# Optimization experiments

Measured on AMD Instinct MI355X. Metric: run time of the kernel, lower is better.

## Reference

```python
import jax, jax.numpy as jnp
import numpy as np

TEXT_VOCAB = 32000
NUM_CODEBOOKS = 8
CODEBOOK_SIZE = 1024
SLICE = CODEBOOK_SIZE + 2  # codebook slice length incl. BOS/EOS
AUDIO_VOCAB = NUM_CODEBOOKS * SLICE  # 8208
HIDDEN = 2048
NH = 16
NKV = 8
HD = HIDDEN // NH  # 128
FFN = 8192
LAYERS = 2
EPS = 1e-5


def setup_inputs() -> dict:
    key = jax.random.key(0)
    ks = jax.random.split(key, 16)
    s = 0.02
    qkv_dim = (NH + 2 * NKV) * HD  # 4096
    inp = {
        "input_ids": jax.random.randint(ks[0], (2, 1024), 0, TEXT_VOCAB + CODEBOOK_SIZE, dtype=jnp.int32),
        "vocab_embed": jax.random.normal(ks[1], (TEXT_VOCAB, HIDDEN), jnp.float32) * s,
        "audio_embed": jax.random.normal(ks[2], (AUDIO_VOCAB, HIDDEN), jnp.float32) * s,
        "ln_in": jnp.ones((LAYERS, HIDDEN), jnp.float32),
        "ln_audio_in": jnp.ones((LAYERS, HIDDEN), jnp.float32),
        "ln_post": jnp.ones((LAYERS, HIDDEN), jnp.float32),
        "ln_audio_post": jnp.ones((LAYERS, HIDDEN), jnp.float32),
        "w_qkv": jax.random.normal(ks[3], (LAYERS, HIDDEN, qkv_dim), jnp.float32) * s,
        "w_o": jax.random.normal(ks[4], (LAYERS, NH * HD, HIDDEN), jnp.float32) * s,
        "w_fc": jax.random.normal(ks[5], (LAYERS, HIDDEN, FFN), jnp.float32) * s,
        "w_proj": jax.random.normal(ks[6], (LAYERS, FFN, HIDDEN), jnp.float32) * s,
        "w_audio_fc": jax.random.normal(ks[7], (LAYERS, HIDDEN, FFN), jnp.float32) * s,
        "w_audio_proj": jax.random.normal(ks[8], (LAYERS, FFN, HIDDEN), jnp.float32) * s,
        "ln_f": jnp.ones((HIDDEN,), jnp.float32),
    }
    return inp


def _rms(x, w):
    return x * jax.lax.rsqrt(jnp.mean(x * x, axis=-1, keepdims=True) + EPS) * w


def reference(input_ids, vocab_embed, audio_embed, ln_in, ln_audio_in, ln_post,
              ln_audio_post, w_qkv, w_o, w_fc, w_proj, w_audio_fc, w_audio_proj, ln_f):
    B, S = input_ids.shape
    audio_mask = input_ids > TEXT_VOCAB - 1  # [B,S] bool
    mask3 = audio_mask[..., None]

    # --- embedding ---
    text_ids = jnp.where(audio_mask, TEXT_VOCAB - 1, input_ids)
    text_e = vocab_embed[text_ids]  # [B,S,H]
    audio_ids = jnp.where(audio_mask, input_ids - TEXT_VOCAB, 0)
    shift = jnp.arange(NUM_CODEBOOKS, dtype=jnp.int32) * SLICE  # [C]
    audio_e = audio_embed[audio_ids[None] + shift[:, None, None]].sum(0)  # [B,S,H]
    h = jnp.where(mask3, audio_e, text_e)

    causal = jnp.tril(jnp.ones((S, S), bool))
    scale = 1.0 / np.sqrt(HD)

    def layer(h, p):
        li, lai, lp, lap, wqkv, wo, wfc, wpr, wafc, wapr = p
        # dual-path input norm (both computed, merged by mask)
        x = jnp.where(mask3, _rms(h, lai), _rms(h, li))
        # causal GQA attention
        qkv = x @ wqkv
        q = qkv[..., : NH * HD].reshape(B, S, NH, HD)
        k = qkv[..., NH * HD:(NH + NKV) * HD].reshape(B, S, NKV, HD)
        v = qkv[..., (NH + NKV) * HD:].reshape(B, S, NKV, HD)
        rep = NH // NKV
        k = jnp.repeat(k, rep, axis=2)
        v = jnp.repeat(v, rep, axis=2)
        scores = jnp.einsum('bqhd,bkhd->bhqk', q, k) * scale
        scores = jnp.where(causal, scores, jnp.finfo(scores.dtype).min)
        attn = jax.nn.softmax(scores, axis=-1)
        o = jnp.einsum('bhqk,bkhd->bqhd', attn, v).reshape(B, S, NH * HD) @ wo
        h = h + o
        # dual-path FFN (both computed, merged by mask)
        y_text = jax.nn.silu(_rms(h, lp) @ wfc) @ wpr
        y_audio = jax.nn.silu(_rms(h, lap) @ wafc) @ wapr
        h = h + jnp.where(mask3, y_audio, y_text)
        return h, None

    params = (ln_in, ln_audio_in, ln_post, ln_audio_post,
              w_qkv, w_o, w_fc, w_proj, w_audio_fc, w_audio_proj)
    h, _ = jax.lax.scan(layer, h, params)
    return _rms(h, ln_f)
```

## Files before the change

### kernel.cpp

```cpp
#include <hip/hip_runtime.h>
#include <hip/hip_bf16.h>

typedef unsigned short u16;
typedef __attribute__((ext_vector_type(4))) float f32x4;
typedef __attribute__((ext_vector_type(8))) short bf16x8;
typedef __attribute__((ext_vector_type(8))) unsigned short u16x8;
typedef __attribute__((ext_vector_type(4))) unsigned short u16x4;

#define BM 128
#define BN 128
#define BK 64

__device__ __forceinline__ u16 f2bf(float f) {
  union { float f; unsigned u; } v; v.f = f;
  unsigned r = v.u + 0x7FFFu + ((v.u >> 16) & 1u);
  return (u16)(r >> 16);
}
__device__ __forceinline__ float bf2f(u16 v) {
  union { float f; unsigned u; } x; x.u = (unsigned)v << 16; return x.f;
}

__device__ __forceinline__ int xswz(int wg, int n) {
  return (wg & 7) * (n >> 3) + (wg >> 3);
}

__device__ __forceinline__ void g8_stage_half(
    const u16* __restrict__ G, int ldg, int tile, int half, u16* ldsbase) {
  const int tid = threadIdx.x;
#pragma unroll
  for (int load = 0; load < 2; ++load) {
    int unit = load * 512 + tid;
    int row = unit >> 3;
    int seg = (unit & 7) ^ ((unit >> 3) & 7);
    __builtin_amdgcn_global_load_lds(
        (const __attribute__((address_space(1))) void*)(G + (size_t)(half * 128 + row) * ldg + tile * 64 + seg * 8),
        (__attribute__((address_space(3))) void*)(ldsbase + half * 8192 + load * 4096 + (tid >> 6) * 512),
        16, 0, 0);
  }
}

__device__ __forceinline__ void g8_core(
    const u16* __restrict__ A, int lda, const u16* __restrict__ Bt, int ldb,
    int NT, u16* lds, f32x4 acc[8][4]) {
  const int tid = threadIdx.x;
  const int lane = tid & 63;
  const int wid = tid >> 6;
  const int wr = wid >> 2, wc = wid & 3;
  const int lr = lane & 15;
  const int lk4 = lane >> 4;
  const int sw = lane & 7;
  const int off0 = ((lk4 ^ sw) * 8);
  const int off1 = (((4 + lk4) ^ sw) * 8);

  u16* ldsA = lds;
  u16* ldsB = lds + 32768;

  g8_stage_half(A, lda, 0, 0, ldsA);
  g8_stage_half(A, lda, 0, 1, ldsA);
  g8_stage_half(Bt, ldb, 0, 0, ldsB);
  g8_stage_half(Bt, ldb, 0, 1, ldsB);
  if (NT > 1) {
    g8_stage_half(Bt, ldb, 1, 0, ldsB + 16384);
    g8_stage_half(Bt, ldb, 1, 1, ldsB + 16384);
  }
  asm volatile("s_waitcnt vmcnt(4)" ::: "memory");
  __builtin_amdgcn_s_barrier();
  __builtin_amdgcn_sched_barrier(0);

  for (int g = 0; g < NT; ++g) {
    const int buf = g & 1;
    const u16* cA = ldsA + buf * 16384 + wr * 8192;
    const u16* cB = ldsB + buf * 16384;
    bf16x8 bv[4][2];
#pragma unroll
    for (int p = 0; p < 4; ++p) {
      bf16x8 av[2][2];
      if (p == 0) {
#pragma unroll
        for (int n = 0; n < 4; ++n) {
          int rg = wc * 64 + n * 16 + lr;
          const u16* rbase = &cB[(rg >> 7) * 8192 + (rg & 127) * 64];
          bv[n][0] = *(const bf16x8*)&rbase[off0];
          bv[n][1] = *(const bf16x8*)&rbase[off1];
        }
      }
#pragma unroll
      for (int m2 = 0; m2 < 2; ++m2) {
        const u16* rbase = &cA[((p * 2 + m2) * 16 + lr) * 64];
        av[m2][0] = *(const bf16x8*)&rbase[off0];
        av[m2][1] = *(const bf16x8*)&rbase[off1];
      }

      if (p == 0 && g + 1 < NT) g8_stage_half(A, lda, g + 1, 0, ldsA + ((g + 1) & 1) * 16384);
      if (p == 1 && g + 1 < NT) g8_stage_half(A, lda, g + 1, 1, ldsA + ((g + 1) & 1) * 16384);
      if (p == 2 && g + 2 < NT) g8_stage_half(Bt, ldb, g + 2, 0, ldsB + buf * 16384);
      if (p == 3) {
        if (g + 2 < NT) {
          g8_stage_half(Bt, ldb, g + 2, 1, ldsB + buf * 16384);
          asm volatile("s_waitcnt vmcnt(4)" ::: "memory");
        } else if (g + 1 < NT) {
          asm volatile("s_waitcnt vmcnt(0)" ::: "memory");
        }
      }
      __builtin_amdgcn_s_barrier();
      asm volatile("s_waitcnt lgkmcnt(0)" ::: "memory");
      __builtin_amdgcn_sched_barrier(0);
      __builtin_amdgcn_s_setprio(1);
#pragma unroll
      for (int m2 = 0; m2 < 2; ++m2)
#pragma unroll
        for (int n = 0; n < 4; ++n)
#pragma unroll
          for (int kk = 0; kk < 2; ++kk)
            acc[p * 2 + m2][n] = __builtin_amdgcn_mfma_f32_16x16x32_bf16(
                av[m2][kk], bv[n][kk], acc[p * 2 + m2][n], 0, 0, 0);
      __builtin_amdgcn_s_setprio(0);
      __builtin_amdgcn_sched_barrier(0);
      __builtin_amdgcn_s_barrier();
    }
  }
}

__device__ __forceinline__ void g8_acc_zero(f32x4 acc[8][4]) {
#pragma unroll
  for (int m = 0; m < 8; ++m)
#pragma unroll
    for (int n = 0; n < 4; ++n)
      acc[m][n] = (f32x4){0.f, 0.f, 0.f, 0.f};
}

__global__ __launch_bounds__(512, 2) void k_gemm8_qkv(
    const u16* __restrict__ A, const u16* __restrict__ Bt, u16* __restrict__ Pq) {
  __shared__ u16 lds[65536];
  const int wg = xswz(blockIdx.x, 256);
  const int ks = wg >> 7, rem = wg & 127;
  const int tm = rem >> 4, tn = rem & 15;
  f32x4 acc[8][4];
  g8_acc_zero(acc);
  g8_core(A + (size_t)tm * 256 * 2048 + ks * 1024, 2048,
          Bt + (size_t)tn * 256 * 2048 + ks * 1024, 2048, 16, lds, acc);
  const int lane = threadIdx.x & 63, wid = threadIdx.x >> 6;
  const int wr = wid >> 2, wc = wid & 3;
  const int col = lane & 15, rb = (lane >> 4) * 4;
#pragma unroll
  for (int m = 0; m < 8; ++m)
#pragma unroll
    for (int n = 0; n < 4; ++n)
#pragma unroll
      for (int j = 0; j < 4; ++j) {
        int gm = tm * 256 + wr * 128 + m * 16 + rb + j;
        int gn = tn * 256 + wc * 64 + n * 16 + col;
        Pq[((size_t)ks * 2048 + gm) * 4096 + gn] = f2bf(acc[m][n][j]);
      }
}

__global__ __launch_bounds__(512, 2) void k_gemm8_fc(
    const u16* __restrict__ A, const u16* __restrict__ Bt, u16* __restrict__ Cb) {
  __shared__ u16 lds[65536];
  const int wg = xswz(blockIdx.x, 256);
  const int tm = wg >> 5, tn = wg & 31;
  f32x4 acc[8][4];
  g8_acc_zero(acc);
  g8_core(A + (size_t)tm * 256 * 2048, 2048, Bt + (size_t)tn * 256 * 2048, 2048, 32, lds, acc);
  const int lane = threadIdx.x & 63, wid = threadIdx.x >> 6;
  const int wr = wid >> 2, wc = wid & 3;
  const int col = lane & 15, rb = (lane >> 4) * 4;
#pragma unroll
  for (int m = 0; m < 8; ++m)
#pragma unroll
    for (int n = 0; n < 4; ++n)
#pragma unroll
      for (int j = 0; j < 4; ++j) {
        int gm = tm * 256 + wr * 128 + m * 16 + rb + j;
        int gn = tn * 256 + wc * 64 + n * 16 + col;
        float v = acc[m][n][j];
        Cb[(size_t)gm * 8192 + gn] = f2bf(v / (1.f + __expf(-v)));
      }
}

__global__ __launch_bounds__(512, 2) void k_gemm8_sk(
    const u16* __restrict__ A, int lda, const u16* __restrict__ Bt, int ldb,
    int NT, int koff, u16* __restrict__ Pp) {
  __shared__ u16 lds[65536];
  const int wg = xswz(blockIdx.x, 256);
  const int ks = wg >> 6, rem = wg & 63;
  const int tm = rem >> 3, tn = rem & 7;
  f32x4 acc[8][4];
  g8_acc_zero(acc);
  g8_core(A + (size_t)tm * 256 * lda + ks * koff, lda,
          Bt + (size_t)tn * 256 * ldb + ks * koff, ldb, NT, lds, acc);
  const int lane = threadIdx.x & 63, wid = threadIdx.x >> 6;
  const int wr = wid >> 2, wc = wid & 3;
  const int col = lane & 15, rb = (lane >> 4) * 4;
#pragma unroll
  for (int m = 0; m < 8; ++m)
#pragma unroll
    for (int n = 0; n < 4; ++n)
#pragma unroll
      for (int j = 0; j < 4; ++j) {
        int gm = tm * 256 + wr * 128 + m * 16 + rb + j;
        int gn = tn * 256 + wc * 64 + n * 16 + col;
        Pp[((size_t)ks * 2048 + gm) * 2048 + gn] = f2bf(acc[m][n][j]);
      }
}

__global__ __launch_bounds__(256) void k_red_qkv(
    const u16* __restrict__ Pq, u16* __restrict__ Q, u16* __restrict__ Kb,
    u16* __restrict__ VT) {
  const int gm = blockIdx.y;
  const int c = blockIdx.x * 1024 + threadIdx.x * 4;
  const size_t i = (size_t)gm * 4096 + c;
  u16x4 a = *(const u16x4*)&Pq[i];
  u16x4 b2 = *(const u16x4*)&Pq[(size_t)2048 * 4096 + i];
  const int b = gm >> 10, s = gm & 1023;
  u16 v[4];
#pragma unroll
  for (int j = 0; j < 4; ++j) v[j] = f2bf(bf2f(a[j]) + bf2f(b2[j]));
  const int d = c & 127;
  if (c < 2048) {
    int hh = c >> 7;
    *(u16x4*)&Q[((size_t)((b * 16 + hh) * 1024 + s)) * 128 + d] = *(u16x4*)v;
  } else if (c < 3072) {
    int kv = (c - 2048) >> 7;
    *(u16x4*)&Kb[((size_t)((b * 8 + kv) * 1024 + s)) * 128 + d] = *(u16x4*)v;
  } else {
    int kv = (c - 3072) >> 7;
#pragma unroll
    for (int j = 0; j < 4; ++j)
      VT[((size_t)((b * 8 + kv) * 128 + d + j)) * 1024 + s] = v[j];
  }
}

__device__ __forceinline__ void fa_stage128(const u16* __restrict__ G, int ldg, u16* dst,
                                            int nloads) {
  const int tid = threadIdx.x;
  for (int ld = 0; ld < nloads; ++ld) {
    int unit = ld * 256 + tid;
    int row = unit >> 4;
    int seg = (unit & 15) ^ (row & 7);
    __builtin_amdgcn_global_load_lds(
        (const __attribute__((address_space(1))) void*)(G + (size_t)row * ldg + seg * 8),
        (__attribute__((address_space(3))) void*)(dst + ld * 2048 + (tid >> 6) * 512),
        16, 0, 0);
  }
}
__device__ __forceinline__ void fa_stage64(const u16* __restrict__ G, int ldg, u16* dst,
                                           int nloads) {
  const int tid = threadIdx.x;
  for (int ld = 0; ld < nloads; ++ld) {
    int unit = ld * 256 + tid;
    int row = unit >> 3;
    int seg = (unit & 7) ^ (row & 7);
    __builtin_amdgcn_global_load_lds(
        (const __attribute__((address_space(1))) void*)(G + (size_t)row * ldg + seg * 8),
        (__attribute__((address_space(3))) void*)(dst + ld * 2048 + (tid >> 6) * 512),
        16, 0, 0);
  }
}

__global__ __launch_bounds__(256, 2) void k_fattn(
    const u16* __restrict__ Q, const u16* __restrict__ Kb, const u16* __restrict__ VT,
    u16* __restrict__ O) {
  const int tm = blockIdx.x;
  const int bh = blockIdx.y;
  const int b = bh >> 4, hq = bh & 15, kv = hq >> 1;
  __shared__ u16 lds[32768];
  u16* Klds = lds;
  u16* Vlds = lds + 8192;
  u16* Plds = lds + 24576;
  const int lane = threadIdx.x & 63, wave = threadIdx.x >> 6;
  const int wm = wave * 32;
  const int lr = lane & 15, lk = lane >> 4;
  const int rb = lk * 4;
  const int cl = lr;

  const u16* Qg = Q + ((size_t)(b * 16 + hq) * 1024 + tm * 128) * 128;
  fa_stage128(Qg, 128, lds, 8);
  asm volatile("s_waitcnt vmcnt(0)" ::: "memory");
  __builtin_amdgcn_s_barrier();
  __builtin_amdgcn_sched_barrier(0);
  bf16x8 qf[2][4];
#pragma unroll
  for (int m = 0; m < 2; ++m)
#pragma unroll
    for (int kk = 0; kk < 4; ++kk) {
      int row = wm + m * 16 + lr;
      qf[m][kk] = *(const bf16x8*)&lds[row * 128 + (((kk * 4 + lk) ^ (lr & 7)) * 8)];
    }
  asm volatile("s_waitcnt lgkmcnt(0)" ::: "memory");
  __builtin_amdgcn_s_barrier();
  __builtin_amdgcn_sched_barrier(0);

  const u16* Kg = Kb + (size_t)(b * 8 + kv) * 1024 * 128;
  const u16* Vg = VT + (size_t)(b * 8 + kv) * 128 * 1024;
  const int NT = 2 * (tm + 1);
  fa_stage128(Kg, 128, Klds, 4);
  fa_stage64(Vg, 1024, Vlds, 4);

  f32x4 accO[2][8];
#pragma unroll
  for (int m = 0; m < 2; ++m)
#pragma unroll
    for (int n = 0; n < 8; ++n) accO[m][n] = (f32x4){0.f, 0.f, 0.f, 0.f};
  float mst[8], lst[8];
#pragma unroll
  for (int i = 0; i < 8; ++i) { mst[i] = -3.0e38f; lst[i] = 0.f; }
  const float scale = 0.08838834764831845f;

  for (int t = 0; t < NT; ++t) {
    asm volatile("s_waitcnt vmcnt(0)" ::: "memory");
    __builtin_amdgcn_s_barrier();
    __builtin_amdgcn_sched_barrier(0);
    u16* Vcur = Vlds + (t & 1) * 8192;
    f32x4 accS[2][4];
#pragma unroll
    for (int m = 0; m < 2; ++m)
#pragma unroll
      for (int n = 0; n < 4; ++n) accS[m][n] = (f32x4){0.f, 0.f, 0.f, 0.f};
#pragma unroll
    for (int kk = 0; kk < 4; ++kk) {
      bf16x8 kf[4];
#pragma unroll
      for (int n = 0; n < 4; ++n)
        kf[n] = *(const bf16x8*)&Klds[(n * 16 + lr) * 128 + (((kk * 4 + lk) ^ (lr & 7)) * 8)];
#pragma unroll
      for (int m = 0; m < 2; ++m)
#pragma unroll
        for (int n = 0; n < 4; ++n)
          accS[m][n] = __builtin_amdgcn_mfma_f32_16x16x32_bf16(qf[m][kk], kf[n], accS[m][n], 0, 0, 0);
    }
    asm volatile("s_waitcnt lgkmcnt(0)" ::: "memory");
    __builtin_amdgcn_s_barrier();
    __builtin_amdgcn_sched_barrier(0);
    if (t + 1 < NT) {
      fa_stage128(Kg + (size_t)(t + 1) * 64 * 128, 128, Klds, 4);
      fa_stage64(Vg + (t + 1) * 64, 1024, Vlds + ((t + 1) & 1) * 8192, 4);
    }
    const bool dm = (t >= 2 * tm);
#pragma unroll
    for (int m = 0; m < 2; ++m)
#pragma unroll
      for (int j = 0; j < 4; ++j) {
        const int si = m * 4 + j;
        const int rglob = tm * 128 + wm + m * 16 + rb + j;
        float v[4];
        float vmax = -3.0e38f;
#pragma unroll
        for (int n = 0; n < 4; ++n) {
          float x = accS[m][n][j] * scale;
          if (dm && (t * 64 + n * 16 + cl > rglob)) x = -3.0e38f;
          v[n] = x;
          vmax = fmaxf(vmax, x);
        }
#pragma unroll
        for (int o = 1; o < 16; o <<= 1) vmax = fmaxf(vmax, __shfl_xor(vmax, o));
        float mnew = fmaxf(mst[si], vmax);
        float alpha = __expf(mst[si] - mnew);
        mst[si] = mnew;
        float rs = 0.f;
        const int prow = wm + m * 16 + rb + j;
#pragma unroll
        for (int n = 0; n < 4; ++n) {
          float pp = __expf(v[n] - mnew);
          rs += pp;
          int col = n * 16 + cl;
          Plds[prow * 64 + (((col >> 3) ^ (prow & 7)) * 8) + (col & 7)] = f2bf(pp);
        }
#pragma unroll
        for (int o = 1; o < 16; o <<= 1) rs += __shfl_xor(rs, o);
        lst[si] = lst[si] * alpha + rs;
#pragma unroll
        for (int n = 0; n < 8; ++n) accO[m][n][j] *= alpha;
      }
#pragma unroll
    for (int kk = 0; kk < 2; ++kk) {
      bf16x8 pf[2], vf[8];
#pragma unroll
      for (int m = 0; m < 2; ++m) {
        int prow = wm + m * 16 + lr;
        pf[m] = *(const bf16x8*)&Plds[prow * 64 + (((kk * 4 + lk) ^ (lr & 7)) * 8)];
      }
#pragma unroll
      for (int n = 0; n < 8; ++n) {
        int d = n * 16 + lr;
        vf[n] = *(const bf16x8*)&Vcur[d * 64 + (((kk * 4 + lk) ^ (d & 7)) * 8)];
      }
#pragma unroll
      for (int m = 0; m < 2; ++m)
#pragma unroll
        for (int n = 0; n < 8; ++n)
          accO[m][n] = __builtin_amdgcn_mfma_f32_16x16x32_bf16(pf[m], vf[n], accO[m][n], 0, 0, 0);
    }
  }
#pragma unroll
  for (int m = 0; m < 2; ++m)
#pragma unroll
    for (int j = 0; j < 4; ++j) {
      float invl = 1.f / lst[m * 4 + j];
      int s = tm * 128 + wm + m * 16 + rb + j;
#pragma unroll
      for (int n = 0; n < 8; ++n) {
        int d = n * 16 + cl;
        O[(size_t)(b * 1024 + s) * 2048 + hq * 128 + d] = f2bf(accO[m][n][j] * invl);
      }
    }
}

__device__ __forceinline__ void acc_zero(f32x4 acc[4][4]) {
#pragma unroll
  for (int m = 0; m < 4; ++m)
#pragma unroll
    for (int n = 0; n < 4; ++n)
      acc[m][n] = (f32x4){0.f, 0.f, 0.f, 0.f};
}

__global__ __launch_bounds__(256) void k_gemm_csf(
    const u16* __restrict__ A, int lda, const float* __restrict__ Wf, int ldw,
    int ksteps, int ntn, u16* __restrict__ Pp, const int* __restrict__ cnt) {
  const int Na = cnt[0];
  const int tm = blockIdx.y;
  if (tm * 128 >= Na) return;
  const int tn = blockIdx.x % ntn;
  const int ks = blockIdx.x / ntn;
  const int ldc = ntn * 128;
  const int k0 = ks * ksteps * BK;
  __shared__ u16 sA[2 * BM * BK], sB[2 * BN * BK];
  f32x4 acc[4][4];
  acc_zero(acc);

  const u16* Ab = A + (size_t)tm * 128 * lda + k0;
  const float* Wb = Wf + (size_t)k0 * ldw + tn * 128;

  const int tid = threadIdx.x;
  const int wave = tid >> 6, lane = tid & 63;
  const int r = tid >> 3;
  const int ksw = (tid & 7) ^ ((tid >> 3) & 7);
  const int wm = (wave >> 1) * 64, wn = (wave & 1) * 64;
  const int lr = lane & 15, lk4 = lane >> 4, sw = lane & 7;
  const int off0 = ((lk4 ^ sw) * 8), off1 = (((4 + lk4) ^ sw) * 8);
  const int amax = Na - 1 - tm * 128;
  const int bk_ = tid >> 5;
  const int bn4 = (tid & 31) * 4;

  f32x4 breg[8];

  auto stageA = [&](int buf, int kt) {
    u16* dA = sA + buf * 8192 + wave * 512;
    const int kk0 = kt * BK;
#pragma unroll
    for (int i = 0; i < 4; ++i) {
      int ra = i * 32 + r; if (ra > amax) ra = amax;
      __builtin_amdgcn_global_load_lds(
          (const __attribute__((address_space(1))) void*)(Ab + (size_t)ra * lda + kk0 + ksw * 8),
          (__attribute__((address_space(3))) void*)(dA + i * 2048), 16, 0, 0);
    }
  };
  auto loadB = [&](int kt) {
#pragma unroll
    for (int i = 0; i < 8; ++i) {
      int kk_ = kt * 64 + i * 8 + bk_;
      breg[i] = __builtin_nontemporal_load((const f32x4*)&Wb[(size_t)kk_ * ldw + bn4]);
    }
  };
  auto writeB = [&](int buf) {
    u16* dB = sB + buf * 8192;
#pragma unroll
    for (int i = 0; i < 8; ++i) {
      int kk_ = i * 8 + bk_;
#pragma unroll
      for (int j = 0; j < 4; ++j) {
        int n = bn4 + j;
        dB[n * 64 + (((kk_ >> 3) ^ (n & 7)) * 8) + (kk_ & 7)] = f2bf(breg[i][j]);
      }
    }
  };

  stageA(0, 0);
  loadB(0);
  asm volatile("s_waitcnt vmcnt(0)" ::: "memory");
  writeB(0);
  asm volatile("s_waitcnt lgkmcnt(0)" ::: "memory");
  __builtin_amdgcn_s_barrier();
  __builtin_amdgcn_sched_barrier(0);

  for (int kt = 0; kt < ksteps; ++kt) {
    const int cur = kt & 1;
    if (kt + 1 < ksteps) { stageA(cur ^ 1, kt + 1); loadB(kt + 1); }
    const u16* cA = sA + cur * 8192;
    const u16* cB = sB + cur * 8192;
#pragma unroll
    for (int kk = 0; kk < 2; ++kk) {
      const int off = kk ? off1 : off0;
      bf16x8 av[4], bv[4];
#pragma unroll
      for (int m = 0; m < 4; ++m)
        av[m] = *(const bf16x8*)&cA[(wm + m * 16 + lr) * BK + off];
#pragma unroll
      for (int n = 0; n < 4; ++n)
        bv[n] = *(const bf16x8*)&cB[(wn + n * 16 + lr) * BK + off];
#pragma unroll
      for (int m = 0; m < 4; ++m)
#pragma unroll
        for (int n = 0; n < 4; ++n)
          acc[m][n] = __builtin_amdgcn_mfma_f32_16x16x32_bf16(av[m], bv[n], acc[m][n], 0, 0, 0);
    }
    asm volatile("s_waitcnt vmcnt(0)" ::: "memory");
    if (kt + 1 < ksteps) writeB(cur ^ 1);
    asm volatile("s_waitcnt lgkmcnt(0)" ::: "memory");
    __builtin_amdgcn_s_barrier();
    __builtin_amdgcn_sched_barrier(0);
  }

  const int col = lane & 15, rb = (lane >> 4) * 4;
#pragma unroll
  for (int m = 0; m < 4; ++m)
#pragma unroll
    for (int n = 0; n < 4; ++n)
#pragma unroll
      for (int j = 0; j < 4; ++j) {
        int gm = tm * 128 + wm + m * 16 + rb + j;
        int gn = tn * 128 + wn + n * 16 + col;
        Pp[((size_t)ks * 256 + gm) * ldc + gn] = f2bf(acc[m][n][j]);
      }
}

__global__ __launch_bounds__(256) void k_red8_silu(
    const u16* __restrict__ Pp, u16* __restrict__ t1, const int* __restrict__ cnt) {
  const int row = blockIdx.y;
  if (row >= cnt[0]) return;
  const int c = blockIdx.x * 1024 + threadIdx.x * 4;
  const size_t i = (size_t)row * 8192 + c;
  float s[4] = {0.f, 0.f, 0.f, 0.f};
#pragma unroll
  for (int k = 0; k < 8; ++k) {
    u16x4 a = *(const u16x4*)&Pp[(size_t)k * 256 * 8192 + i];
#pragma unroll
    for (int j = 0; j < 4; ++j) s[j] += bf2f(a[j]);
  }
  u16x4 ov;
#pragma unroll
  for (int j = 0; j < 4; ++j) {
    float v = s[j];
    ov[j] = f2bf(v / (1.f + __expf(-v)));
  }
  *(u16x4*)&t1[i] = ov;
}

__device__ __forceinline__ float block_sum256(float v, float* red) {
  const int tid = threadIdx.x;
#pragma unroll
  for (int o = 32; o; o >>= 1) v += __shfl_xor(v, o);
  if ((tid & 63) == 0) red[tid >> 6] = v;
  __syncthreads();
  float r = red[0] + red[1] + red[2] + red[3];
  __syncthreads();
  return r;
}

__global__ __launch_bounds__(256) void k_trans_embed(
    const float* __restrict__ w_qkv, const float* __restrict__ w_o,
    const float* __restrict__ w_fc, const float* __restrict__ w_proj,
    u16* __restrict__ WtAll,
    const int* __restrict__ ids, const float* __restrict__ vocab,
    const float* __restrict__ audio, const float* __restrict__ wt,
    const float* __restrict__ wa, float* __restrict__ h, int* __restrict__ mask,
    u16* __restrict__ x) {
  __shared__ float tile[64][65];
  const int tid = threadIdx.x;
  if (blockIdx.x < 22528) {
    int bid = blockIdx.x;
    int l = 0;
    if (bid >= 11264) { l = 1; bid -= 11264; }
    const float* src;
    u16* dst;
    int K, N, t;
    u16* WtL = WtAll + (size_t)l * 46137344;
    if (bid < 2048)       { src = w_qkv  + (size_t)l * 8388608;  dst = WtL;            K = 2048; N = 4096; t = bid; }
    else if (bid < 3072)  { src = w_o    + (size_t)l * 4194304;  dst = WtL + 8388608;  K = 2048; N = 2048; t = bid - 2048; }
    else if (bid < 7168)  { src = w_fc   + (size_t)l * 16777216; dst = WtL + 12582912; K = 2048; N = 8192; t = bid - 3072; }
    else                  { src = w_proj + (size_t)l * 16777216; dst = WtL + 29360128; K = 8192; N = 2048; t = bid - 7168; }
    const int nk = K >> 6;
    const int sb = t >> 6, w = t & 63;
    const int nsbk = nk >> 3;
    const int tk = ((sb % nsbk) << 3) + (w & 7);
    const int tn = ((sb / nsbk) << 3) + (w >> 3);
#pragma unroll
    for (int i = 0; i < 4; ++i) {
      int idx = i * 256 + tid;
      int r = idx >> 4, c4 = (idx & 15) * 4;
      f32x4 v = __builtin_nontemporal_load(
          (const f32x4*)&src[(size_t)(tk * 64 + r) * N + tn * 64 + c4]);
      tile[r][c4]     = v[0];
      tile[r][c4 + 1] = v[1];
      tile[r][c4 + 2] = v[2];
      tile[r][c4 + 3] = v[3];
    }
    __syncthreads();
#pragma unroll
    for (int i = 0; i < 2; ++i) {
      int u = i * 256 + tid;
      int n = u >> 3, seg = u & 7;
      u16x8 ov;
#pragma unroll
      for (int j = 0; j < 8; ++j) ov[j] = f2bf(tile[seg * 8 + j][n]);
      __builtin_nontemporal_store(ov,
          (u16x8*)&dst[(size_t)(tn * 64 + n) * K + tk * 64 + seg * 8]);
    }
  } else {
    const int t = blockIdx.x - 22528;
    const int id = ids[t];
    const int am = (id > 31999) ? 1 : 0;
    if (tid == 0) mask[t] = am;
    float* hr = h + (size_t)t * 2048;
    const int c0 = tid * 8;
    float4 v0, v1;
    if (!am) {
      const float4* src = (const float4*)(vocab + (size_t)id * 2048);
      v0 = src[tid * 2];
      v1 = src[tid * 2 + 1];
    } else {
      const int aid = id - 32000;
      v0 = (float4){0.f, 0.f, 0.f, 0.f};
      v1 = (float4){0.f, 0.f, 0.f, 0.f};
#pragma unroll
      for (int c = 0; c < 8; ++c) {
        const float4* ap = (const float4*)(audio + (size_t)(aid + c * 1026) * 2048);
        float4 a0 = ap[tid * 2], a1 = ap[tid * 2 + 1];
        v0.x += a0.x; v0.y += a0.y; v0.z += a0.z; v0.w += a0.w;
        v1.x += a1.x; v1.y += a1.y; v1.z += a1.z; v1.w += a1.w;
      }
    }
    ((float4*)hr)[tid * 2] = v0;
    ((float4*)hr)[tid * 2 + 1] = v1;
    const float* f0 = (const float*)&v0;
    const float* f1 = (const float*)&v1;
    float ss = 0.f;
#pragma unroll
    for (int j = 0; j < 4; ++j) ss += f0[j] * f0[j] + f1[j] * f1[j];
    float* red = &tile[0][0];
    ss = block_sum256(ss, red);
    const float inv = rsqrtf(ss * (1.0f / 2048.0f) + 1e-5f);
    const float* w = am ? wa : wt;
    u16x8 a;
#pragma unroll
    for (int j = 0; j < 8; ++j) {
      float hv = (j < 4 ? f0[j] : f1[j - 4]) * inv;
      a[j] = f2bf(hv * w[c0 + j]);
    }
    *(u16x8*)&x[(size_t)t * 2048 + c0] = a;
  }
}

__global__ __launch_bounds__(256) void k_scan(
    const int* __restrict__ mask, int* __restrict__ cpos,
    int* __restrict__ cidx, int* __restrict__ cnt) {
  const int tid = threadIdx.x;
  const int lane = tid & 63, wid = tid >> 6;
  int m[8];
  int s = 0;
#pragma unroll
  for (int j = 0; j < 8; ++j) { m[j] = mask[tid * 8 + j]; s += m[j]; }
  int ps = s;
#pragma unroll
  for (int o = 1; o < 64; o <<= 1) {
    int t = __shfl_up(ps, o);
    if (lane >= o) ps += t;
  }
  __shared__ int wsum[4];
  if (lane == 63) wsum[wid] = ps;
  __syncthreads();
  int base = 0;
  for (int w = 0; w < wid; ++w) base += wsum[w];
  int run = base + ps - s;
#pragma unroll
  for (int j = 0; j < 8; ++j) {
    int row = tid * 8 + j;
    cpos[row] = run;
    if (m[j]) cidx[run] = row;
    run += m[j];
  }
  if (tid == 255) cnt[0] = run;
}

__global__ __launch_bounds__(256) void k_redrms_post(
    float* __restrict__ h, const u16* __restrict__ Pp,
    const float* __restrict__ wt, const float* __restrict__ wa,
    const int* __restrict__ mask, u16* __restrict__ x, u16* __restrict__ xc,
    const int* __restrict__ cpos) {
  const int row = blockIdx.x, tid = threadIdx.x;
  const int c0 = tid * 8;
  const size_t base = (size_t)row * 2048 + c0;
  float4 a0 = *(const float4*)&h[base];
  float4 a1 = *(const float4*)&h[base + 4];
  float* fa0 = (float*)&a0;
  float* fa1 = (float*)&a1;
#pragma unroll
  for (int k = 0; k < 4; ++k) {
    u16x8 pv = *(const u16x8*)&Pp[(size_t)k * 2048 * 2048 + base];
#pragma unroll
    for (int j = 0; j < 4; ++j) fa0[j] += bf2f(pv[j]);
#pragma unroll
    for (int j = 0; j < 4; ++j) fa1[j] += bf2f(pv[4 + j]);
  }
  *(float4*)&h[base] = a0;
  *(float4*)&h[base + 4] = a1;
  float ss = 0.f;
#pragma unroll
  for (int j = 0; j < 4; ++j) ss += fa0[j] * fa0[j] + fa1[j] * fa1[j];
  __shared__ float red[4];
  ss = block_sum256(ss, red);
  const float inv = rsqrtf(ss * (1.0f / 2048.0f) + 1e-5f);
  u16x8 xv;
#pragma unroll
  for (int j = 0; j < 8; ++j) {
    float hv = (j < 4 ? fa0[j] : fa1[j - 4]) * inv;
    xv[j] = f2bf(hv * wt[c0 + j]);
  }
  *(u16x8*)&x[base] = xv;
  if (mask[row]) {
    u16x8 av;
#pragma unroll
    for (int j = 0; j < 8; ++j) {
      float hv = (j < 4 ? fa0[j] : fa1[j - 4]) * inv;
      av[j] = f2bf(hv * wa[c0 + j]);
    }
    *(u16x8*)&xc[(size_t)cpos[row] * 2048 + c0] = av;
  }
}

__global__ __launch_bounds__(256) void k_redrms_ffn(
    float* __restrict__ h, const u16* __restrict__ Psk, const u16* __restrict__ Pap,
    const float* __restrict__ wt, const float* __restrict__ wa,
    const float* __restrict__ wf, const int* __restrict__ mask,
    const int* __restrict__ cpos, u16* __restrict__ x, float* __restrict__ outf, int fin) {
  const int row = blockIdx.x, tid = threadIdx.x;
  const int c0 = tid * 8;
  const size_t base = (size_t)row * 2048 + c0;
  float4 a0 = *(const float4*)&h[base];
  float4 a1 = *(const float4*)&h[base + 4];
  float* fa0 = (float*)&a0;
  float* fa1 = (float*)&a1;
  if (mask[row] == 0) {
#pragma unroll
    for (int k = 0; k < 4; ++k) {
      u16x8 pv = *(const u16x8*)&Psk[(size_t)k * 2048 * 2048 + base];
#pragma unroll
      for (int j = 0; j < 4; ++j) fa0[j] += bf2f(pv[j]);
#pragma unroll
      for (int j = 0; j < 4; ++j) fa1[j] += bf2f(pv[4 + j]);
    }
  } else {
    const size_t cb = (size_t)cpos[row] * 2048 + c0;
#pragma unroll
    for (int k = 0; k < 16; ++k) {
      u16x8 pv = *(const u16x8*)&Pap[(size_t)k * 256 * 2048 + cb];
#pragma unroll
      for (int j = 0; j < 4; ++j) fa0[j] += bf2f(pv[j]);
#pragma unroll
      for (int j = 0; j < 4; ++j) fa1[j] += bf2f(pv[4 + j]);
    }
  }
  if (!fin) {
    *(float4*)&h[base] = a0;
    *(float4*)&h[base + 4] = a1;
  }
  float ss = 0.f;
#pragma unroll
  for (int j = 0; j < 4; ++j) ss += fa0[j] * fa0[j] + fa1[j] * fa1[j];
  __shared__ float red[4];
  ss = block_sum256(ss, red);
  const float inv = rsqrtf(ss * (1.0f / 2048.0f) + 1e-5f);
  if (fin) {
    float4 o0, o1;
    float* p0 = (float*)&o0;
    float* p1 = (float*)&o1;
#pragma unroll
    for (int j = 0; j < 4; ++j) {
      p0[j] = fa0[j] * inv * wf[c0 + j];
      p1[j] = fa1[j] * inv * wf[c0 + 4 + j];
    }
    *(float4*)&outf[base] = o0;
    *(float4*)&outf[base + 4] = o1;
  } else {
    const float* w = mask[row] ? wa : wt;
    u16x8 xv;
#pragma unroll
    for (int j = 0; j < 8; ++j) {
      float hv = (j < 4 ? fa0[j] : fa1[j - 4]) * inv;
      xv[j] = f2bf(hv * w[c0 + j]);
    }
    *(u16x8*)&x[base] = xv;
  }
}

extern "C" void kernel_launch(void* const* d_in, const int* in_sizes, int n_in,
                              void* d_out, int out_size, void* d_ws, size_t ws_size,
                              hipStream_t stream) {
  const int* ids = (const int*)d_in[0];
  const float* vocab = (const float*)d_in[1];
  const float* audio = (const float*)d_in[2];
  const float* ln_in = (const float*)d_in[3];
  const float* ln_audio_in = (const float*)d_in[4];
  const float* ln_post = (const float*)d_in[5];
  const float* ln_audio_post = (const float*)d_in[6];
  const float* w_qkv = (const float*)d_in[7];
  const float* w_o = (const float*)d_in[8];
  const float* w_fc = (const float*)d_in[9];
  const float* w_proj = (const float*)d_in[10];
  const float* w_afc = (const float*)d_in[11];
  const float* w_aproj = (const float*)d_in[12];
  const float* ln_f = (const float*)d_in[13];
  float* out = (float*)d_out;

  char* p = (char*)d_ws;
  auto alloc = [&](size_t bytes) {
    char* r = p;
    p += (bytes + 255) & ~(size_t)255;
    return r;
  };
  float* h   = (float*)alloc((size_t)2048 * 2048 * 4);
  u16* x     = (u16*)alloc((size_t)2048 * 2048 * 2);
  u16* xc    = (u16*)alloc((size_t)2048 * 2048 * 2);
  u16* o     = (u16*)alloc((size_t)2048 * 2048 * 2);
  int* mask  = (int*)alloc((size_t)2048 * 4);
  int* cpos  = (int*)alloc((size_t)2048 * 4);
  int* cidx  = (int*)alloc((size_t)2048 * 4);
  int* cnt   = (int*)alloc((size_t)64 * 4);
  u16* WtAll = (u16*)alloc((size_t)2 * 46137344 * 2);
  u16* Q     = (u16*)alloc((size_t)2 * 16 * 1024 * 128 * 2);
  u16* Kb    = (u16*)alloc((size_t)2 * 8 * 1024 * 128 * 2);
  u16* VT    = (u16*)alloc((size_t)2 * 8 * 1024 * 128 * 2);
  char* A    = alloc((size_t)128 * 1024 * 1024);
  char* Bg   = alloc((size_t)24 * 1024 * 1024);
  u16* t1    = (u16*)alloc((size_t)2048 * 8192 * 2);
  u16* Pq    = (u16*)A;
  u16* Psk   = (u16*)A;
  u16* Pafc  = (u16*)(A + (size_t)67108864);
  u16* Paprj = (u16*)Bg;
  (void)ws_size; (void)in_sizes; (void)n_in; (void)out_size;

  k_trans_embed<<<24576, 256, 0, stream>>>(w_qkv, w_o, w_fc, w_proj, WtAll,
                                           ids, vocab, audio, ln_in, ln_audio_in, h, mask, x);
  k_scan<<<1, 256, 0, stream>>>(mask, cpos, cidx, cnt);

  for (int l = 0; l < 2; ++l) {
    u16* WtL = WtAll + (size_t)l * 46137344;
    u16* Wqkv_t  = WtL;
    u16* Wo_t    = WtL + 8388608;
    u16* Wfc_t   = WtL + 12582912;
    u16* Wproj_t = WtL + 29360128;

    k_gemm8_qkv<<<256, 512, 0, stream>>>(x, Wqkv_t, Pq);
    k_red_qkv<<<dim3(4, 2048), 256, 0, stream>>>(Pq, Q, Kb, VT);
    k_fattn<<<dim3(8, 32), 256, 0, stream>>>(Q, Kb, VT, o);
    k_gemm8_sk<<<256, 512, 0, stream>>>(o, 2048, Wo_t, 2048, 8, 512, Psk);
    k_redrms_post<<<2048, 256, 0, stream>>>(h, Psk, ln_post + l * 2048,
                                            ln_audio_post + l * 2048, mask, x, xc, cpos);
    k_gemm8_fc<<<256, 512, 0, stream>>>(x, Wfc_t, t1);
    k_gemm8_sk<<<256, 512, 0, stream>>>(t1, 8192, Wproj_t, 8192, 32, 2048, Psk);
    k_gemm_csf<<<dim3(64 * 8, 2), 256, 0, stream>>>(
        xc, 2048, w_afc + (size_t)l * 2048 * 8192, 8192, 4, 64, Pafc, cnt);
    k_red8_silu<<<dim3(8, 256), 256, 0, stream>>>(Pafc, t1, cnt);
    k_gemm_csf<<<dim3(16 * 16, 2), 256, 0, stream>>>(
        t1, 8192, w_aproj + (size_t)l * 8192 * 2048, 2048, 8, 16, Paprj, cnt);
    if (l == 0)
      k_redrms_ffn<<<2048, 256, 0, stream>>>(h, Psk, Paprj, ln_in + 2048,
                                             ln_audio_in + 2048, nullptr, mask, cpos, x,
                                             nullptr, 0);
    else
      k_redrms_ffn<<<2048, 256, 0, stream>>>(h, Psk, Paprj, nullptr, nullptr, ln_f, mask,
                                             cpos, nullptr, out, 1);
  }
}
```

Baseline: 896.2 us.

## Co-launch text FFN GEMMs with compacted audio FFN GEMMs in shared grids

Merges the text FC GEMM with the audio FC split-K GEMM, and the text projection GEMM with the audio projection GEMM, into single launches. Extra blocks in each grid take the audio path through a 512-thread body in which only 4 waves compute and all 8 help stage data. A separate t1a buffer holds the audio intermediate so the two paths no longer share t1. The aim is to cut launch count and fill idle CUs by running the small audio GEMMs alongside the large text ones, at the cost of idle waves in audio blocks and mixed block shapes.

Result: faster. 876.5 us (-2.2%).

```diff
diff --git a/kernel.cpp b/kernel.cpp
--- a/kernel.cpp
+++ b/kernel.cpp
@@ -6,10 +6,6 @@
 typedef __attribute__((ext_vector_type(8))) short bf16x8;
 typedef __attribute__((ext_vector_type(8))) unsigned short u16x8;
 typedef __attribute__((ext_vector_type(4))) unsigned short u16x4;
-
-#define BM 128
-#define BN 128
-#define BK 64
 
 __device__ __forceinline__ u16 f2bf(float f) {
   union { float f; unsigned u; } v; v.f = f;
@@ -127,6 +123,113 @@
 #pragma unroll
     for (int n = 0; n < 4; ++n)
       acc[m][n] = (f32x4){0.f, 0.f, 0.f, 0.f};
+}
+
+__device__ __forceinline__ void acc_zero4(f32x4 acc[4][4]) {
+#pragma unroll
+  for (int m = 0; m < 4; ++m)
+#pragma unroll
+    for (int n = 0; n < 4; ++n)
+      acc[m][n] = (f32x4){0.f, 0.f, 0.f, 0.f};
+}
+
+__device__ __forceinline__ void csf512_body(
+    const u16* __restrict__ Ab, int lda, const float* __restrict__ Wb, int ldw,
+    int ksteps, int amax, u16* lds, u16* __restrict__ Pout, int ldc) {
+  u16* sA = lds;
+  u16* sB = lds + 16384;
+  const int tid = threadIdx.x;
+  const int wave = tid >> 6, lane = tid & 63;
+  const int lr = lane & 15, lk4 = lane >> 4, sw = lane & 7;
+  const int off0 = ((lk4 ^ sw) * 8), off1 = (((4 + lk4) ^ sw) * 8);
+  const int srow = tid >> 3;
+  const int ssw = (tid & 7) ^ ((tid >> 3) & 7);
+  const int kb = tid >> 5;
+  const int bn4 = (tid & 31) * 4;
+  f32x4 breg[4];
+
+  auto stageA = [&](int buf, int kt) {
+    const int kk0 = kt * 64;
+#pragma unroll
+    for (int i = 0; i < 2; ++i) {
+      int ra = i * 64 + srow; if (ra > amax) ra = amax;
+      __builtin_amdgcn_global_load_lds(
+          (const __attribute__((address_space(1))) void*)(Ab + (size_t)ra * lda + kk0 + ssw * 8),
+          (__attribute__((address_space(3))) void*)(sA + buf * 8192 + i * 4096 + wave * 512),
+          16, 0, 0);
+    }
+  };
+  auto loadB = [&](int kt) {
+#pragma unroll
+    for (int i = 0; i < 4; ++i) {
+      int kk = kt * 64 + i * 16 + kb;
+      breg[i] = __builtin_nontemporal_load((const f32x4*)&Wb[(size_t)kk * ldw + bn4]);
+    }
+  };
+  auto writeB = [&](int buf) {
+    u16* dB = sB + buf * 8192;
+#pragma unroll
+    for (int i = 0; i < 4; ++i) {
+      int kk = i * 16 + kb;
+#pragma unroll
+      for (int j = 0; j < 4; ++j) {
+        int n = bn4 + j;
+        dB[n * 64 + (((kk >> 3) ^ (n & 7)) * 8) + (kk & 7)] = f2bf(breg[i][j]);
+      }
+    }
+  };
+
+  f32x4 acc[4][4];
+  acc_zero4(acc);
+
+  stageA(0, 0);
+  loadB(0);
+  asm volatile("s_waitcnt vmcnt(0)" ::: "memory");
+  writeB(0);
+  asm volatile("s_waitcnt lgkmcnt(0)" ::: "memory");
+  __builtin_amdgcn_s_barrier();
+  __builtin_amdgcn_sched_barrier(0);
+
+  const int wm = (wave >> 1) * 64, wn = (wave & 1) * 64;
+  for (int kt = 0; kt < ksteps; ++kt) {
+    const int cur = kt & 1;
+    if (kt + 1 < ksteps) { stageA(cur ^ 1, kt + 1); loadB(kt + 1); }
+    if (wave < 4) {
+      const u16* cA = sA + cur * 8192;
+      const u16* cB = sB + cur * 8192;
+#pragma unroll
+      for (int kk = 0; kk < 2; ++kk) {
+        const int off = kk ? off1 : off0;
+        bf16x8 av[4], bv[4];
+#pragma unroll
+        for (int m = 0; m < 4; ++m)
+          av[m] = *(const bf16x8*)&cA[(wm + m * 16 + lr) * 64 + off];
+#pragma unroll
+        for (int n = 0; n < 4; ++n)
+          bv[n] = *(const bf16x8*)&cB[(wn + n * 16 + lr) * 64 + off];
+#pragma unroll
+        for (int m = 0; m < 4; ++m)
+#pragma unroll
+          for (int n = 0; n < 4; ++n)
+            acc[m][n] = __builtin_amdgcn_mfma_f32_16x16x32_bf16(av[m], bv[n], acc[m][n], 0, 0, 0);
+      }
+    }
+    asm volatile("s_waitcnt vmcnt(0)" ::: "memory");
+    if (kt + 1 < ksteps) writeB(cur ^ 1);
+    asm volatile("s_waitcnt lgkmcnt(0)" ::: "memory");
+    __builtin_amdgcn_s_barrier();
+    __builtin_amdgcn_sched_barrier(0);
+  }
+  if (wave < 4) {
+    const int col = lane & 15, rb = (lane >> 4) * 4;
+#pragma unroll
+    for (int m = 0; m < 4; ++m)
+#pragma unroll
+      for (int n = 0; n < 4; ++n)
+#pragma unroll
+        for (int j = 0; j < 4; ++j)
+          Pout[(size_t)(wm + m * 16 + rb + j) * ldc + wn + n * 16 + col] = f2bf(acc[m][n][j]);
+  }
 }
 
 __global__ __launch_bounds__(512, 2) void k_gemm8_qkv(
@@ -151,30 +254,6 @@
         int gm = tm * 256 + wr * 128 + m * 16 + rb + j;
         int gn = tn * 256 + wc * 64 + n * 16 + col;
         Pq[((size_t)ks * 2048 + gm) * 4096 + gn] = f2bf(acc[m][n][j]);
-      }
-}
-
-__global__ __launch_bounds__(512, 2) void k_gemm8_fc(
-    const u16* __restrict__ A, const u16* __restrict__ Bt, u16* __restrict__ Cb) {
-  __shared__ u16 lds[65536];
-  const int wg = xswz(blockIdx.x, 256);
-  const int tm = wg >> 5, tn = wg & 31;
-  f32x4 acc[8][4];
-  g8_acc_zero(acc);
-  g8_core(A + (size_t)tm * 256 * 2048, 2048, Bt + (size_t)tn * 256 * 2048, 2048, 32, lds, acc);
-  const int lane = threadIdx.x & 63, wid = threadIdx.x >> 6;
-  const int wr = wid >> 2, wc = wid & 3;
-  const int col = lane & 15, rb = (lane >> 4) * 4;
-#pragma unroll
-  for (int m = 0; m < 8; ++m)
-#pragma unroll
-    for (int n = 0; n < 4; ++n)
-#pragma unroll
-      for (int j = 0; j < 4; ++j) {
-        int gm = tm * 256 + wr * 128 + m * 16 + rb + j;
-        int gn = tn * 256 + wc * 64 + n * 16 + col;
-        float v = acc[m][n][j];
-        Cb[(size_t)gm * 8192 + gn] = f2bf(v / (1.f + __expf(-v)));
       }
 }
 
@@ -202,6 +281,83 @@
         int gn = tn * 256 + wc * 64 + n * 16 + col;
         Pp[((size_t)ks * 2048 + gm) * 2048 + gn] = f2bf(acc[m][n][j]);
       }
+}
+
+__global__ __launch_bounds__(512, 2) void k_fc_afc(
+    const u16* __restrict__ A, const u16* __restrict__ Bt, u16* __restrict__ Cb,
+    const u16* __restrict__ xc, const float* __restrict__ w_afc,
+    u16* __restrict__ Pafc, const int* __restrict__ cnt) {
+  __shared__ u16 lds[65536];
+  if (blockIdx.x < 256) {
+    const int wg = xswz(blockIdx.x, 256);
+    const int tm = wg >> 5, tn = wg & 31;
+    f32x4 acc[8][4];
+    g8_acc_zero(acc);
+    g8_core(A + (size_t)tm * 256 * 2048, 2048, Bt + (size_t)tn * 256 * 2048, 2048, 32, lds, acc);
+    const int lane = threadIdx.x & 63, wid = threadIdx.x >> 6;
+    const int wr = wid >> 2, wc = wid & 3;
+    const int col = lane & 15, rb = (lane >> 4) * 4;
+#pragma unroll
+    for (int m = 0; m < 8; ++m)
+#pragma unroll
+      for (int n = 0; n < 4; ++n)
+#pragma unroll
+        for (int j = 0; j < 4; ++j) {
+          int gm = tm * 256 + wr * 128 + m * 16 + rb + j;
+          int gn = tn * 256 + wc * 64 + n * 16 + col;
+          float v = acc[m][n][j];
+          Cb[(size_t)gm * 8192 + gn] = f2bf(v / (1.f + __expf(-v)));
+        }
+  } else {
+    const int a = blockIdx.x - 256;
+    const int tm = a >> 9, r = a & 511, tn = r & 63, ks = r >> 6;
+    const int Na = cnt[0];
+    if (tm * 128 >= Na) return;
+    const int k0 = ks * 256;
+    csf512_body(xc + (size_t)tm * 128 * 2048 + k0, 2048,
+                w_afc + (size_t)k0 * 8192 + tn * 128, 8192,
+                4, Na - 1 - tm * 128, lds,
+                Pafc + ((size_t)ks * 256 + tm * 128) * 8192 + tn * 128, 8192);
+  }
+}
+
+__global__ __launch_bounds__(512, 2) void k_sk_aproj(
+    const u16* __restrict__ A, const u16* __restrict__ Bt, u16* __restrict__ Psk,
+    const u16* __restrict__ t1a, const float* __restrict__ w_aproj,
+    u16* __restrict__ Paprj, const int* __restrict__ cnt) {
+  __shared__ u16 lds[65536];
+  if (blockIdx.x < 256) {
+    const int wg = xswz(blockIdx.x, 256);
+    const int ks = wg >> 6, rem = wg & 63;
+    const int tm = rem >> 3, tn = rem & 7;
+    f32x4 acc[8][4];
+    g8_acc_zero(acc);
+    g8_core(A + (size_t)tm * 256 * 8192 + ks * 2048, 8192,
+            Bt + (size_t)tn * 256 * 8192 + ks * 2048, 8192, 32, lds, acc);
+    const int lane = threadIdx.x & 63, wid = threadIdx.x >> 6;
+    const int wr = wid >> 2, wc = wid & 3;
+    const int col = lane & 15, rb = (lane >> 4) * 4;
+#pragma unroll
+    for (int m = 0; m < 8; ++m)
+#pragma unroll
+      for (int n = 0; n < 4; ++n)
+#pragma unroll
+        for (int j = 0; j < 4; ++j) {
+          int gm = tm * 256 + wr * 128 + m * 16 + rb + j;
+          int gn = tn * 256 + wc * 64 + n * 16 + col;
+          Psk[((size_t)ks * 2048 + gm) * 2048 + gn] = f2bf(acc[m][n][j]);
+        }
+  } else {
+    const int a = blockIdx.x - 256;
+    const int tm = a >> 8, r = a & 255, tn = r & 15, ks = r >> 4;
+    const int Na = cnt[0];
+    if (tm * 128 >= Na) return;
+    const int k0 = ks * 512;
+    csf512_body(t1a + (size_t)tm * 128 * 8192 + k0, 8192,
+                w_aproj + (size_t)k0 * 2048 + tn * 128, 2048,
+                8, Na - 1 - tm * 128, lds,
+                Paprj + ((size_t)ks * 256 + tm * 128) * 2048 + tn * 128, 2048);
+  }
 }
 
 __global__ __launch_bounds__(256) void k_red_qkv(
@@ -406,126 +562,8 @@
     }
 }
 
-__device__ __forceinline__ void acc_zero(f32x4 acc[4][4]) {
-#pragma unroll
-  for (int m = 0; m < 4; ++m)
-#pragma unroll
-    for (int n = 0; n < 4; ++n)
-      acc[m][n] = (f32x4){0.f, 0.f, 0.f, 0.f};
-}
-
-__global__ __launch_bounds__(256) void k_gemm_csf(
-    const u16* __restrict__ A, int lda, const float* __restrict__ Wf, int ldw,
-    int ksteps, int ntn, u16* __restrict__ Pp, const int* __restrict__ cnt) {
-  const int Na = cnt[0];
-  const int tm = blockIdx.y;
-  if (tm * 128 >= Na) return;
-  const int tn = blockIdx.x % ntn;
-  const int ks = blockIdx.x / ntn;
-  const int ldc = ntn * 128;
-  const int k0 = ks * ksteps * BK;
-  __shared__ u16 sA[2 * BM * BK], sB[2 * BN * BK];
-  f32x4 acc[4][4];
-  acc_zero(acc);
-
-  const u16* Ab = A + (size_t)tm * 128 * lda + k0;
-  const float* Wb = Wf + (size_t)k0 * ldw + tn * 128;
-
-  const int tid = threadIdx.x;
-  const int wave = tid >> 6, lane = tid & 63;
-  const int r = tid >> 3;
-  const int ksw = (tid & 7) ^ ((tid >> 3) & 7);
-  const int wm = (wave >> 1) * 64, wn = (wave & 1) * 64;
-  const int lr = lane & 15, lk4 = lane >> 4, sw = lane & 7;
-  const int off0 = ((lk4 ^ sw) * 8), off1 = (((4 + lk4) ^ sw) * 8);
-  const int amax = Na - 1 - tm * 128;
-  const int bk_ = tid >> 5;
-  const int bn4 = (tid & 31) * 4;
-
-  f32x4 breg[8];
-
-  auto stageA = [&](int buf, int kt) {
-    u16* dA = sA + buf * 8192 + wave * 512;
-    const int kk0 = kt * BK;
-#pragma unroll
-    for (int i = 0; i < 4; ++i) {
-      int ra = i * 32 + r; if (ra > amax) ra = amax;
-      __builtin_amdgcn_global_load_lds(
-          (const __attribute__((address_space(1))) void*)(Ab + (size_t)ra * lda + kk0 + ksw * 8),
-          (__attribute__((address_space(3))) void*)(dA + i * 2048), 16, 0, 0);
-    }
-  };
-  auto loadB = [&](int kt) {
-#pragma unroll
-    for (int i = 0; i < 8; ++i) {
-      int kk_ = kt * 64 + i * 8 + bk_;
-      breg[i] = __builtin_nontemporal_load((const f32x4*)&Wb[(size_t)kk_ * ldw + bn4]);
-    }
-  };
-  auto writeB = [&](int buf) {
-    u16* dB = sB + buf * 8192;
-#pragma unroll
-    for (int i = 0; i < 8; ++i) {
-      int kk_ = i * 8 + bk_;
-#pragma unroll
-      for (int j = 0; j < 4; ++j) {
-        int n = bn4 + j;
-        dB[n * 64 + (((kk_ >> 3) ^ (n & 7)) * 8) + (kk_ & 7)] = f2bf(breg[i][j]);
-      }
-    }
-  };
-
-  stageA(0, 0);
-  loadB(0);
-  asm volatile("s_waitcnt vmcnt(0)" ::: "memory");
-  writeB(0);
-  asm volatile("s_waitcnt lgkmcnt(0)" ::: "memory");
-  __builtin_amdgcn_s_barrier();
-  __builtin_amdgcn_sched_barrier(0);
-
-  for (int kt = 0; kt < ksteps; ++kt) {
-    const int cur = kt & 1;
-    if (kt + 1 < ksteps) { stageA(cur ^ 1, kt + 1); loadB(kt + 1); }
-    const u16* cA = sA + cur * 8192;
-    const u16* cB = sB + cur * 8192;
-#pragma unroll
-    for (int kk = 0; kk < 2; ++kk) {
-      const int off = kk ? off1 : off0;
-      bf16x8 av[4], bv[4];
-#pragma unroll
-      for (int m = 0; m < 4; ++m)
-        av[m] = *(const bf16x8*)&cA[(wm + m * 16 + lr) * BK + off];
-#pragma unroll
-      for (int n = 0; n < 4; ++n)
-        bv[n] = *(const bf16x8*)&cB[(wn + n * 16 + lr) * BK + off];
-#pragma unroll
-      for (int m = 0; m < 4; ++m)
-#pragma unroll
-        for (int n = 0; n < 4; ++n)
-          acc[m][n] = __builtin_amdgcn_mfma_f32_16x16x32_bf16(av[m], bv[n], acc[m][n], 0, 0, 0);
-    }
-    asm volatile("s_waitcnt vmcnt(0)" ::: "memory");
-    if (kt + 1 < ksteps) writeB(cur ^ 1);
-    asm volatile("s_waitcnt lgkmcnt(0)" ::: "memory");
-    __builtin_amdgcn_s_barrier();
-    __builtin_amdgcn_sched_barrier(0);
-  }
-
-  const int col = lane & 15, rb = (lane >> 4) * 4;
-#pragma unroll
-  for (int m = 0; m < 4; ++m)
-#pragma unroll
-    for (int n = 0; n < 4; ++n)
-#pragma unroll
-      for (int j = 0; j < 4; ++j) {
-        int gm = tm * 128 + wm + m * 16 + rb + j;
-        int gn = tn * 128 + wn + n * 16 + col;
-        Pp[((size_t)ks * 256 + gm) * ldc + gn] = f2bf(acc[m][n][j]);
-      }
-}
-
 __global__ __launch_bounds__(256) void k_red8_silu(
-    const u16* __restrict__ Pp, u16* __restrict__ t1, const int* __restrict__ cnt) {
+    const u16* __restrict__ Pp, u16* __restrict__ t1a, const int* __restrict__ cnt) {
   const int row = blockIdx.y;
   if (row >= cnt[0]) return;
   const int c = blockIdx.x * 1024 + threadIdx.x * 4;
@@ -543,7 +581,7 @@
     float v = s[j];
     ov[j] = f2bf(v / (1.f + __expf(-v)));
   }
-  *(u16x4*)&t1[i] = ov;
+  *(u16x4*)&t1a[i] = ov;
 }
 
 __device__ __forceinline__ float block_sum256(float v, float* red) {
@@ -833,6 +871,7 @@
   char* A    = alloc((size_t)128 * 1024 * 1024);
   char* Bg   = alloc((size_t)24 * 1024 * 1024);
   u16* t1    = (u16*)alloc((size_t)2048 * 8192 * 2);
+  u16* t1a   = (u16*)alloc((size_t)256 * 8192 * 2);
   u16* Pq    = (u16*)A;
   u16* Psk   = (u16*)A;
   u16* Pafc  = (u16*)(A + (size_t)67108864);
@@ -856,13 +895,11 @@
     k_gemm8_sk<<<256, 512, 0, stream>>>(o, 2048, Wo_t, 2048, 8, 512, Psk);
     k_redrms_post<<<2048, 256, 0, stream>>>(h, Psk, ln_post + l * 2048,
                                             ln_audio_post + l * 2048, mask, x, xc, cpos);
-    k_gemm8_fc<<<256, 512, 0, stream>>>(x, Wfc_t, t1);
-    k_gemm8_sk<<<256, 512, 0, stream>>>(t1, 8192, Wproj_t, 8192, 32, 2048, Psk);
-    k_gemm_csf<<<dim3(64 * 8, 2), 256, 0, stream>>>(
-        xc, 2048, w_afc + (size_t)l * 2048 * 8192, 8192, 4, 64, Pafc, cnt);
-    k_red8_silu<<<dim3(8, 256), 256, 0, stream>>>(Pafc, t1, cnt);
-    k_gemm_csf<<<dim3(16 * 16, 2), 256, 0, stream>>>(
-        t1, 8192, w_aproj + (size_t)l * 8192 * 2048, 2048, 8, 16, Paprj, cnt);
+    k_fc_afc<<<1280, 512, 0, stream>>>(x, Wfc_t, t1, xc,
+                                       w_afc + (size_t)l * 2048 * 8192, Pafc, cnt);
+    k_red8_silu<<<dim3(8, 256), 256, 0, stream>>>(Pafc, t1a, cnt);
+    k_sk_aproj<<<768, 512, 0, stream>>>(t1, Wproj_t, Psk, t1a,
+                                        w_aproj + (size_t)l * 8192 * 2048, Paprj, cnt);
     if (l == 0)
       k_redrms_ffn<<<2048, 256, 0, stream>>>(h, Psk, Paprj, ln_in + 2048,
                                              ln_audio_in + 2048, nullptr, mask, cpos, x,
```
